# Kernel optimization log

Measured on AMD Instinct MI355X. Metric: run time of the kernel, lower is better.

## Reference

```python
import jax, jax.numpy as jnp
import numpy as np

NUM_GROUPS = 4
KERNEL_SIZE = 3


def _conv1x1(x, w, b):
    # x: [B,Cin,H,W], w: [Cout,Cin], b: [Cout]
    return jnp.einsum('bchw,oc->bohw', x, w) + b[None, :, None, None]


def _unfold(t, ks):
    # t: [B,G,Gd,H,W] -> patches [B,G,Gd,ks*ks,H,W] with zero padding (pad=ks//2)
    pad = ks // 2
    H, W = t.shape[-2:]
    tp = jnp.pad(t, ((0, 0), (0, 0), (0, 0), (pad, pad), (pad, pad)))
    return jnp.stack([tp[..., i:i + H, j:j + W]
                      for i in range(ks) for j in range(ks)], axis=3)


def setup_inputs() -> dict:
    key = jax.random.key(0)
    ks = jax.random.split(key, 7)
    B, Cin, C, H, W = 4, 256, 256, 64, 64
    s = 1.0 / np.sqrt(Cin)
    return {
        'x': jax.random.normal(ks[0], (B, Cin, H, W), dtype=jnp.float32),
        'wq': jax.random.normal(ks[1], (C, Cin), dtype=jnp.float32) * s,
        'bq': jax.random.normal(ks[2], (C,), dtype=jnp.float32) * 0.01,
        'wk': jax.random.normal(ks[3], (C, Cin), dtype=jnp.float32) * s,
        'bk': jax.random.normal(ks[4], (C,), dtype=jnp.float32) * 0.01,
        'wv': jax.random.normal(ks[5], (C, Cin), dtype=jnp.float32) * s,
        'bv': jax.random.normal(ks[6], (C,), dtype=jnp.float32) * 0.01,
    }


def reference(x, wq, bq, wk, bk, wv, bv):
    B, _, H, W = x.shape
    C = wq.shape[0]
    G = NUM_GROUPS
    Gd = C // G
    q = _conv1x1(x, wq, bq).reshape(B, G, Gd, H, W)
    k = _conv1x1(x, wk, bk).reshape(B, G, Gd, H, W)
    v = _conv1x1(x, wv, bv).reshape(B, G, Gd, H, W)
    kp = _unfold(k, KERNEL_SIZE)  # [B,G,Gd,k2,H,W]
    vp = _unfold(v, KERNEL_SIZE)  # [B,G,Gd,k2,H,W]
    attn = jnp.einsum('bgdhw,bgdphw->bgphw', q, kp)  # [B,G,k2,H,W]
    attn = jax.nn.softmax(attn, axis=2)
    out = jnp.einsum('bgphw,bgdphw->bgdhw', attn, vp)  # [B,G,Gd,H,W]
    return out.reshape(B, C, H, W)
```

## Files before the change

### kernel.cpp

```cpp
#include <hip/hip_runtime.h>
#include <cstddef>
#include <cstdint>

#define BDIM 4
#define HH   64
#define WW   64
#define NG   4
#define GD   64
#define HWSZ 4096
#define NTOT 16384
#define XTC  256

typedef __attribute__((ext_vector_type(4))) float f32x4;
typedef _Float16 f16x4_t __attribute__((ext_vector_type(4)));
typedef _Float16 f16x8_t __attribute__((ext_vector_type(8)));

__device__ __forceinline__ void lds_load16(const void* g, void* l) {
    __builtin_amdgcn_global_load_lds(
        (const __attribute__((address_space(1))) unsigned int*)g,
        (__attribute__((address_space(3))) unsigned int*)l, 16, 0, 0);
}

__global__ __launch_bounds__(256) void prep_kernel(
    const float* __restrict__ x,
    const float* __restrict__ wq, const float* __restrict__ bq,
    const float* __restrict__ wk, const float* __restrict__ bk,
    const float* __restrict__ wv, const float* __restrict__ bv,
    _Float16* __restrict__ xt, _Float16* __restrict__ Ap,
    float* __restrict__ biasC)
{
    __shared__ float tile[64][65];
    const int t = threadIdx.x;
    const int bx = blockIdx.x;

    if (bx < 1024) {
        const int n0 = (bx & 63) * 64;
        const int c0 = ((bx >> 6) & 3) * 64;
        const int b  = bx >> 8;

        const int tr = t >> 4, tc = (t & 15) * 4;
        #pragma unroll
        for (int i = 0; i < 4; ++i) {
            const int row = tr + i * 16;
            const float4 v = *(const float4*)&x[(size_t)(b * 256 + c0 + row) * HWSZ + n0 + tc];
            tile[row][tc + 0] = v.x; tile[row][tc + 1] = v.y;
            tile[row][tc + 2] = v.z; tile[row][tc + 3] = v.w;
        }
        __syncthreads();

        const int nr = t >> 2, cc = (t & 3) * 16;
        f16x8_t h0, h1;
        #pragma unroll
        for (int j = 0; j < 8; ++j) h0[j] = (_Float16)tile[cc + j][nr];
        #pragma unroll
        for (int j = 0; j < 8; ++j) h1[j] = (_Float16)tile[cc + 8 + j][nr];
        const size_t base = (size_t)(b * HWSZ + n0 + nr) * XTC + c0 + cc;
        *(f16x8_t*)&xt[base]     = h0;
        *(f16x8_t*)&xt[base + 8] = h1;
    } else {
        const int m  = bx - 1024;
        const int mm = m & 255;
        const float* w = (m < 256) ? wq : (m < 512) ? wk : wv;
        Ap[(size_t)m * XTC + t] = (_Float16)w[(size_t)mm * 256 + t];
        if (t == 0) biasC[m] = (m < 256) ? bq[mm] : (m < 512) ? bk[mm] : bv[mm];
    }
}

__global__ __launch_bounds__(256) void qkv_mfma_kernel(
    const _Float16* __restrict__ Ap, const _Float16* __restrict__ xt,
    const float* __restrict__ biasC, _Float16* __restrict__ qh,
    _Float16* __restrict__ kh, _Float16* __restrict__ vh)
{
    __shared__ _Float16 As[128 * 32];
    __shared__ _Float16 Bs[128 * 32];

    const int t  = threadIdx.x;
    const int bx = blockIdx.x;
    const int u  = (bx & 7) * 96 + (bx >> 3);
    const int mt = u % 6;
    const int nt = u / 6;

    const int l     = t & 63;
    const int wid   = t >> 6;
    const int wm    = wid >> 1, wn = wid & 1;
    const int lrow  = l & 15;
    const int lk    = (l >> 4) * 8;
    const int lrow4 = (l >> 4) * 4;

    f32x4 acc[4][4];
    #pragma unroll
    for (int mi = 0; mi < 4; ++mi) {
        const f32x4 bb = *(const f32x4*)&biasC[mt * 128 + wm * 64 + mi * 16 + lrow4];
        #pragma unroll
        for (int ni = 0; ni < 4; ++ni) acc[mi][ni] = bb;
    }

    const int e  = t * 8;
    const int r0 = e >> 5;
    const int kc = e & 31;
    const _Float16* agp0 = Ap + (size_t)(mt * 128 + r0) * XTC + kc;
    const _Float16* agp1 = Ap + (size_t)(mt * 128 + 64 + r0) * XTC + kc;
    const _Float16* bgp0 = xt + (size_t)(nt * 128 + r0) * XTC + kc;
    const _Float16* bgp1 = xt + (size_t)(nt * 128 + 64 + r0) * XTC + kc;

    for (int kt = 0; kt < 8; ++kt) {
        const int ka = kt * 32;
        lds_load16(agp0 + ka, As + t * 8);
        lds_load16(agp1 + ka, As + 2048 + t * 8);
        lds_load16(bgp0 + ka, Bs + t * 8);
        lds_load16(bgp1 + ka, Bs + 2048 + t * 8);
        __syncthreads();

        f16x8_t a[4], bf[4];
        #pragma unroll
        for (int mi = 0; mi < 4; ++mi)
            a[mi] = *(const f16x8_t*)&As[(wm * 64 + mi * 16 + lrow) * 32 + lk];
        #pragma unroll
        for (int ni = 0; ni < 4; ++ni)
            bf[ni] = *(const f16x8_t*)&Bs[(wn * 64 + ni * 16 + lrow) * 32 + lk];
        #pragma unroll
        for (int mi = 0; mi < 4; ++mi)
            #pragma unroll
            for (int ni = 0; ni < 4; ++ni)
                acc[mi][ni] = __builtin_amdgcn_mfma_f32_16x16x32_f16(
                    a[mi], bf[ni], acc[mi][ni], 0, 0, 0);
        __syncthreads();
    }

    #pragma unroll
    for (int ni = 0; ni < 4; ++ni) {
        const size_t ng = (size_t)(nt * 128 + wn * 64 + ni * 16 + lrow);
        #pragma unroll
        for (int mi = 0; mi < 4; ++mi) {
            f16x4_t hv;
            #pragma unroll
            for (int j = 0; j < 4; ++j) hv[j] = (_Float16)acc[mi][ni][j];
            const int c8 = wm * 4 + mi;
            if (mt < 2)
                *(f16x4_t*)&qh[((size_t)(mt * 8 + c8) * NTOT + ng) * 16 + lrow4] = hv;
            else if (mt < 4)
                *(f16x4_t*)&kh[((size_t)((mt - 2) * 8 + c8) * NTOT + ng) * 16 + lrow4] = hv;
            else
                *(f16x4_t*)&vh[((size_t)((mt - 4) * 8 + c8) * NTOT + ng) * 16 + lrow4] = hv;
        }
    }
}

__global__ __launch_bounds__(256) void loc_attn_kernel(
    const _Float16* __restrict__ qh, const _Float16* __restrict__ kh,
    const _Float16* __restrict__ vh, float* __restrict__ out)
{
    const int t   = threadIdx.x;
    const int bx0 = blockIdx.x;
    const int bx  = (bx0 & 7) * 128 + (bx0 >> 3);
    const int h = bx & 63;
    const int g = (bx >> 6) & 3;
    const int b = bx >> 8;

    const int wl  = t & 15;
    const int c   = (t >> 4) & 3;
    const int wid = t >> 6;
    const int w   = wid * 16 + wl;

    const int ck = g * 4 + c;
    const size_t n = (size_t)b * HWSZ + h * 64 + w;

    float qf[16];
    {
        const _Float16* qp = &qh[((size_t)ck * NTOT + n) * 16];
        const f16x8_t q0 = *(const f16x8_t*)qp;
        const f16x8_t q1 = *(const f16x8_t*)(qp + 8);
        #pragma unroll
        for (int j = 0; j < 8; ++j) { qf[j] = (float)q0[j]; qf[8 + j] = (float)q1[j]; }
    }

    float logit[9];
    #pragma unroll
    for (int p = 0; p < 9; ++p) {
        const int dh = p / 3 - 1, dw = p % 3 - 1;
        const int hh = h + dh, ww2 = w + dw;
        float part = 0.f;
        if (hh >= 0 && hh < HH && ww2 >= 0 && ww2 < WW) {
            const size_t nn = (size_t)b * HWSZ + hh * 64 + ww2;
            const _Float16* kp = &kh[((size_t)ck * NTOT + nn) * 16];
            const f16x8_t k0 = *(const f16x8_t*)kp;
            const f16x8_t k1 = *(const f16x8_t*)(kp + 8);
            #pragma unroll
            for (int j = 0; j < 8; ++j)
                part += qf[j] * (float)k0[j] + qf[8 + j] * (float)k1[j];
        }
        part += __shfl_xor(part, 16, 64);
        part += __shfl_xor(part, 32, 64);
        logit[p] = part;
    }

    float mx = logit[0];
    #pragma unroll
    for (int p = 1; p < 9; ++p) mx = fmaxf(mx, logit[p]);
    float a[9];
    float s = 0.f;
    #pragma unroll
    for (int p = 0; p < 9; ++p) { a[p] = __expf(logit[p] - mx); s += a[p]; }
    const float inv = 1.f / s;
    #pragma unroll
    for (int p = 0; p < 9; ++p) a[p] *= inv;

    float acc[16];
    #pragma unroll
    for (int dd = 0; dd < 16; ++dd) acc[dd] = 0.f;
    #pragma unroll
    for (int p = 0; p < 9; ++p) {
        const int dh = p / 3 - 1, dw = p % 3 - 1;
        const int hh = h + dh, ww2 = w + dw;
        if (hh < 0 || hh >= HH || ww2 < 0 || ww2 >= WW) continue;
        const size_t nn = (size_t)b * HWSZ + hh * 64 + ww2;
        const _Float16* vp = &vh[((size_t)ck * NTOT + nn) * 16];
        const f16x8_t v0 = *(const f16x8_t*)vp;
        const f16x8_t v1 = *(const f16x8_t*)(vp + 8);
        const float ap = a[p];
        #pragma unroll
        for (int j = 0; j < 8; ++j) {
            acc[j]     += ap * (float)v0[j];
            acc[8 + j] += ap * (float)v1[j];
        }
    }

    const int obase = b * 256 + g * 64 + c * 16;
    const int off = h * 64 + w;
    #pragma unroll
    for (int dd = 0; dd < 16; ++dd)
        out[(size_t)(obase + dd) * HWSZ + off] = acc[dd];
}

extern "C" void kernel_launch(void* const* d_in, const int* in_sizes, int n_in,
                              void* d_out, int out_size, void* d_ws, size_t ws_size,
                              hipStream_t stream) {
    const float* x  = (const float*)d_in[0];
    const float* wq = (const float*)d_in[1];
    const float* bq = (const float*)d_in[2];
    const float* wk = (const float*)d_in[3];
    const float* bk = (const float*)d_in[4];
    const float* wv = (const float*)d_in[5];
    const float* bv = (const float*)d_in[6];
    float* out = (float*)d_out;

    char* ws = (char*)d_ws;
    _Float16* qh    = (_Float16*)ws;
    _Float16* kh    = (_Float16*)(ws + 8388608);
    _Float16* vh    = (_Float16*)(ws + 16777216);
    _Float16* xt    = (_Float16*)(ws + 25165824);
    _Float16* Ap    = (_Float16*)(ws + 33554432);
    float*    biasC = (float*)(ws + 33947648);

    prep_kernel<<<dim3(1792), 256, 0, stream>>>(x, wq, bq, wk, bk, wv, bv, xt, Ap, biasC);
    qkv_mfma_kernel<<<dim3(768), 256, 0, stream>>>(Ap, xt, biasC, qh, kh, vh);
    loc_attn_kernel<<<dim3(1024), 256, 0, stream>>>(qh, kh, vh, out);
}
```

Measured before the change: 35.93 us.

## Fuse fp32-to-fp16 prep into QKV GEMM with direct global fragment loads

Removes the separate prep kernel that transposed x and converted weights and biases into fp16 workspace buffers. The QKV GEMM now reads fp32 x and weights straight from global memory into registers, converts them in place, and drops LDS staging and barriers. This saves one launch and a full round trip of x through memory. In exchange, x is read as strided scalar loads (8 loads of stride HWSZ per fragment), and each wave re-reads its tiles with no LDS sharing, which raises global and L2 traffic.

Measured after the change: 58.20 us. +62.0%, slower.

```diff
diff --git a/kernel.cpp b/kernel.cpp
--- a/kernel.cpp
+++ b/kernel.cpp
@@ -9,71 +9,19 @@
 #define GD   64
 #define HWSZ 4096
 #define NTOT 16384
-#define XTC  256
 
 typedef __attribute__((ext_vector_type(4))) float f32x4;
 typedef _Float16 f16x4_t __attribute__((ext_vector_type(4)));
 typedef _Float16 f16x8_t __attribute__((ext_vector_type(8)));
 
-__device__ __forceinline__ void lds_load16(const void* g, void* l) {
-    __builtin_amdgcn_global_load_lds(
-        (const __attribute__((address_space(1))) unsigned int*)g,
-        (__attribute__((address_space(3))) unsigned int*)l, 16, 0, 0);
-}
-
-__global__ __launch_bounds__(256) void prep_kernel(
+__global__ __launch_bounds__(256, 2) void qkv_fused_kernel(
     const float* __restrict__ x,
     const float* __restrict__ wq, const float* __restrict__ bq,
     const float* __restrict__ wk, const float* __restrict__ bk,
     const float* __restrict__ wv, const float* __restrict__ bv,
-    _Float16* __restrict__ xt, _Float16* __restrict__ Ap,
-    float* __restrict__ biasC)
+    _Float16* __restrict__ qh, _Float16* __restrict__ kh,
+    _Float16* __restrict__ vh)
 {
-    __shared__ float tile[64][65];
-    const int t = threadIdx.x;
-    const int bx = blockIdx.x;
-
-    if (bx < 1024) {
-        const int n0 = (bx & 63) * 64;
-        const int c0 = ((bx >> 6) & 3) * 64;
-        const int b  = bx >> 8;
-
-        const int tr = t >> 4, tc = (t & 15) * 4;
-        #pragma unroll
-        for (int i = 0; i < 4; ++i) {
-            const int row = tr + i * 16;
-            const float4 v = *(const float4*)&x[(size_t)(b * 256 + c0 + row) * HWSZ + n0 + tc];
-            tile[row][tc + 0] = v.x; tile[row][tc + 1] = v.y;
-            tile[row][tc + 2] = v.z; tile[row][tc + 3] = v.w;
-        }
-        __syncthreads();
-
-        const int nr = t >> 2, cc = (t & 3) * 16;
-        f16x8_t h0, h1;
-        #pragma unroll
-        for (int j = 0; j < 8; ++j) h0[j] = (_Float16)tile[cc + j][nr];
-        #pragma unroll
-        for (int j = 0; j < 8; ++j) h1[j] = (_Float16)tile[cc + 8 + j][nr];
-        const size_t base = (size_t)(b * HWSZ + n0 + nr) * XTC + c0 + cc;
-        *(f16x8_t*)&xt[base]     = h0;
-        *(f16x8_t*)&xt[base + 8] = h1;
-    } else {
-        const int m  = bx - 1024;
-        const int mm = m & 255;
-        const float* w = (m < 256) ? wq : (m < 512) ? wk : wv;
-        Ap[(size_t)m * XTC + t] = (_Float16)w[(size_t)mm * 256 + t];
-        if (t == 0) biasC[m] = (m < 256) ? bq[mm] : (m < 512) ? bk[mm] : bv[mm];
-    }
-}
-
-__global__ __launch_bounds__(256) void qkv_mfma_kernel(
-    const _Float16* __restrict__ Ap, const _Float16* __restrict__ xt,
-    const float* __restrict__ biasC, _Float16* __restrict__ qh,
-    _Float16* __restrict__ kh, _Float16* __restrict__ vh)
-{
-    __shared__ _Float16 As[128 * 32];
-    __shared__ _Float16 Bs[128 * 32];
-
     const int t  = threadIdx.x;
     const int bx = blockIdx.x;
     const int u  = (bx & 7) * 96 + (bx >> 3);
@@ -84,47 +32,60 @@
     const int wid   = t >> 6;
     const int wm    = wid >> 1, wn = wid & 1;
     const int lrow  = l & 15;
-    const int lk    = (l >> 4) * 8;
+    const int lk8   = (l >> 4) * 8;
     const int lrow4 = (l >> 4) * 4;
 
+    const float* wsel = (mt < 2) ? wq : (mt < 4) ? wk : wv;
+    const float* bsel = (mt < 2) ? bq : (mt < 4) ? bk : bv;
+    _Float16*    osel = (mt < 2) ? qh : (mt < 4) ? kh : vh;
+    const int    mtl  = mt & 1;
+
+    const int n0 = nt * 128 + wn * 64 + lrow;
+    const int bi = n0 >> 12;
+    const int px = n0 & 4095;
+    const float* xb = x + (size_t)bi * 256 * HWSZ + px;
+
     f32x4 acc[4][4];
     #pragma unroll
     for (int mi = 0; mi < 4; ++mi) {
-        const f32x4 bb = *(const f32x4*)&biasC[mt * 128 + wm * 64 + mi * 16 + lrow4];
+        const f32x4 bb = *(const f32x4*)&bsel[mtl * 128 + wm * 64 + mi * 16 + lrow4];
         #pragma unroll
         for (int ni = 0; ni < 4; ++ni) acc[mi][ni] = bb;
     }
 
-    const int e  = t * 8;
-    const int r0 = e >> 5;
-    const int kc = e & 31;
-    const _Float16* agp0 = Ap + (size_t)(mt * 128 + r0) * XTC + kc;
-    const _Float16* agp1 = Ap + (size_t)(mt * 128 + 64 + r0) * XTC + kc;
-    const _Float16* bgp0 = xt + (size_t)(nt * 128 + r0) * XTC + kc;
-    const _Float16* bgp1 = xt + (size_t)(nt * 128 + 64 + r0) * XTC + kc;
-
     for (int kt = 0; kt < 8; ++kt) {
-        const int ka = kt * 32;
-        lds_load16(agp0 + ka, As + t * 8);
-        lds_load16(agp1 + ka, As + 2048 + t * 8);
-        lds_load16(bgp0 + ka, Bs + t * 8);
-        lds_load16(bgp1 + ka, Bs + 2048 + t * 8);
-        __syncthreads();
-
-        f16x8_t a[4], bf[4];
-        #pragma unroll
-        for (int mi = 0; mi < 4; ++mi)
-            a[mi] = *(const f16x8_t*)&As[(wm * 64 + mi * 16 + lrow) * 32 + lk];
-        #pragma unroll
-        for (int ni = 0; ni < 4; ++ni)
-            bf[ni] = *(const f16x8_t*)&Bs[(wn * 64 + ni * 16 + lrow) * 32 + lk];
+        const int k0 = kt * 32 + lk8;
+
+        f16x8_t af[4];
+        #pragma unroll
+        for (int mi = 0; mi < 4; ++mi) {
+            const float* ap = wsel + (size_t)(mtl * 128 + wm * 64 + mi * 16 + lrow) * 256 + k0;
+            const float4 a0 = *(const float4*)ap;
+            const float4 a1 = *(const float4*)(ap + 4);
+            f16x8_t f;
+            f[0] = (_Float16)a0.x; f[1] = (_Float16)a0.y;
+            f[2] = (_Float16)a0.z; f[3] = (_Float16)a0.w;
+            f[4] = (_Float16)a1.x; f[5] = (_Float16)a1.y;
+            f[6] = (_Float16)a1.z; f[7] = (_Float16)a1.w;
+            af[mi] = f;
+        }
+
+        f16x8_t bf[4];
+        #pragma unroll
+        for (int ni = 0; ni < 4; ++ni) {
+            const float* bp = xb + (size_t)k0 * HWSZ + ni * 16;
+            f16x8_t f;
+            #pragma unroll
+            for (int j = 0; j < 8; ++j) f[j] = (_Float16)bp[(size_t)j * HWSZ];
+            bf[ni] = f;
+        }
+
         #pragma unroll
         for (int mi = 0; mi < 4; ++mi)
             #pragma unroll
             for (int ni = 0; ni < 4; ++ni)
                 acc[mi][ni] = __builtin_amdgcn_mfma_f32_16x16x32_f16(
-                    a[mi], bf[ni], acc[mi][ni], 0, 0, 0);
-        __syncthreads();
+                    af[mi], bf[ni], acc[mi][ni], 0, 0, 0);
     }
 
     #pragma unroll
@@ -135,13 +96,8 @@
             f16x4_t hv;
             #pragma unroll
             for (int j = 0; j < 4; ++j) hv[j] = (_Float16)acc[mi][ni][j];
-            const int c8 = wm * 4 + mi;
-            if (mt < 2)
-                *(f16x4_t*)&qh[((size_t)(mt * 8 + c8) * NTOT + ng) * 16 + lrow4] = hv;
-            else if (mt < 4)
-                *(f16x4_t*)&kh[((size_t)((mt - 2) * 8 + c8) * NTOT + ng) * 16 + lrow4] = hv;
-            else
-                *(f16x4_t*)&vh[((size_t)((mt - 4) * 8 + c8) * NTOT + ng) * 16 + lrow4] = hv;
+            const int chunk = mtl * 8 + wm * 4 + mi;
+            *(f16x4_t*)&osel[((size_t)chunk * NTOT + ng) * 16 + lrow4] = hv;
         }
     }
 }
@@ -245,14 +201,11 @@
     float* out = (float*)d_out;
 
     char* ws = (char*)d_ws;
-    _Float16* qh    = (_Float16*)ws;
-    _Float16* kh    = (_Float16*)(ws + 8388608);
-    _Float16* vh    = (_Float16*)(ws + 16777216);
-    _Float16* xt    = (_Float16*)(ws + 25165824);
-    _Float16* Ap    = (_Float16*)(ws + 33554432);
-    float*    biasC = (float*)(ws + 33947648);
-
-    prep_kernel<<<dim3(1792), 256, 0, stream>>>(x, wq, bq, wk, bk, wv, bv, xt, Ap, biasC);
-    qkv_mfma_kernel<<<dim3(768), 256, 0, stream>>>(Ap, xt, biasC, qh, kh, vh);
+    _Float16* qh = (_Float16*)ws;
+    _Float16* kh = (_Float16*)(ws + 8388608);
+    _Float16* vh = (_Float16*)(ws + 16777216);
+
+    qkv_fused_kernel<<<dim3(768), 256, 0, stream>>>(x, wq, bq, wk, bk, wv, bv,
+                                                    qh, kh, vh);
     loc_attn_kernel<<<dim3(1024), 256, 0, stream>>>(qh, kh, vh, out);
 }
```
